# Performance work log

Measured on AMD Instinct MI355X. Metric: run time of the kernel, lower is better.

Reference implementation:

```python
import jax, jax.numpy as jnp
import numpy as np

N = 50000      # nodes
E = 800000     # edges (before self loops)
IN = 128       # in_channels
H = 4          # heads
C = 32         # hidden_channels (per head)
D = H * C      # concat output dim = 128
NEG_SLOPE = 0.2
LN_EPS = 1e-5


def setup_inputs() -> dict:
    key = jax.random.key(0)
    ks = jax.random.split(key, 24)
    def p(k, shape, s=0.1):
        return jax.random.normal(k, shape, dtype=jnp.float32) * s
    inp = {
        "x": p(ks[0], (N, IN), 1.0),
        "edge_index": jax.random.randint(ks[1], (2, E), 0, N, dtype=jnp.int32),
    }
    i = 2
    for l, ind in [(0, IN), (1, D)]:
        inp[f"Wl{l}"] = p(ks[i], (ind, D)); i += 1
        inp[f"bl{l}"] = p(ks[i], (D,), 0.02); i += 1
        inp[f"Wr{l}"] = p(ks[i], (ind, D)); i += 1
        inp[f"br{l}"] = p(ks[i], (D,), 0.02); i += 1
        inp[f"att{l}"] = p(ks[i], (H, C)); i += 1
        inp[f"Wres{l}"] = p(ks[i], (ind, D)); i += 1
        inp[f"bias{l}"] = p(ks[i], (D,), 0.02); i += 1
        inp[f"g{l}"] = jnp.ones((D,), jnp.float32)
        inp[f"be{l}"] = jnp.zeros((D,), jnp.float32)
    return inp


def _gatv2_layer(x, src, dst, Wl, bl, Wr, br, att, Wres, bias):
    """GATv2Conv with concat heads, add_self_loops already applied, residual."""
    n = x.shape[0]
    xl = (x @ Wl + bl).reshape(n, H, C)   # source transform
    xr = (x @ Wr + br).reshape(n, H, C)   # target transform
    # edge-level attention logits: e = a . LeakyReLU(xl[j] + xr[i])  [E, H]
    eh = jax.nn.leaky_relu(xl[src] + xr[dst], negative_slope=NEG_SLOPE)  # [E,H,C]
    score = jnp.einsum('ehc,hc->eh', eh, att)                            # [E,H]
    # segment softmax over incoming edges of each destination node
    smax = jax.ops.segment_max(score, dst, num_segments=n)               # [N,H]
    ex = jnp.exp(score - smax[dst])
    ssum = jax.ops.segment_sum(ex, dst, num_segments=n)                  # [N,H]
    alpha = ex / ssum[dst]                                               # [E,H]
    msg = xl[src] * alpha[:, :, None]                                    # [E,H,C]
    out = jax.ops.segment_sum(msg, dst, num_segments=n).reshape(n, D)
    return out + x @ Wres + bias  # residual (bias=False linear) + final bias


def _layernorm_relu(x, g, b):
    mu = jnp.mean(x, axis=-1, keepdims=True)
    var = jnp.mean(jnp.square(x - mu), axis=-1, keepdims=True)
    return jax.nn.relu((x - mu) * jax.lax.rsqrt(var + LN_EPS) * g + b)


def reference(x, edge_index,
              Wl0, bl0, Wr0, br0, att0, Wres0, bias0, g0, be0,
              Wl1, bl1, Wr1, br1, att1, Wres1, bias1, g1, be1):
    n = x.shape[0]
    loops = jnp.arange(n, dtype=edge_index.dtype)
    src = jnp.concatenate([edge_index[0], loops])  # add_self_loops=True
    dst = jnp.concatenate([edge_index[1], loops])
    h = _gatv2_layer(x, src, dst, Wl0, bl0, Wr0, br0, att0, Wres0, bias0)
    h = _layernorm_relu(h, g0, be0)
    h = _gatv2_layer(h, src, dst, Wl1, bl1, Wr1, br1, att1, Wres1, bias1)
    h = _layernorm_relu(h, g1, be1)
    return h
```

## Files before the change

### kernel.cpp

```cpp
#include <hip/hip_runtime.h>
#include <math.h>

#define D 128
#define LRELU 0.2f
#define LN_EPS 1e-5f
#define INV_LN2 1.4426950408889634f

#define NBMAX 512
#define CAP 4096
#define P1CHUNK 8192

typedef __attribute__((ext_vector_type(8))) short short8;
typedef __attribute__((ext_vector_type(8))) unsigned short ushort8;
typedef __attribute__((ext_vector_type(4))) float f32x4;
typedef __attribute__((ext_vector_type(2))) float f32x2;
typedef __attribute__((ext_vector_type(2))) unsigned int u32x2;

static __device__ __forceinline__ unsigned short f2bf(float f) {
    union { float f; unsigned u; } a; a.f = f;
    unsigned r = a.u + 0x7FFFu + ((a.u >> 16) & 1u);
    return (unsigned short)(r >> 16);
}

static __device__ __forceinline__ f32x2 pk_add(f32x2 a, f32x2 b) {
    f32x2 d; asm("v_pk_add_f32 %0, %1, %2" : "=v"(d) : "v"(a), "v"(b)); return d;
}
static __device__ __forceinline__ f32x2 pk_mul(f32x2 a, f32x2 b) {
    f32x2 d; asm("v_pk_mul_f32 %0, %1, %2" : "=v"(d) : "v"(a), "v"(b)); return d;
}
static __device__ __forceinline__ f32x2 pk_fma(f32x2 a, f32x2 b, f32x2 c) {
    f32x2 d; asm("v_pk_fma_f32 %0, %1, %2, %3" : "=v"(d) : "v"(a), "v"(b), "v"(c)); return d;
}
static __device__ __forceinline__ f32x2 pk_abs(f32x2 a) {
    u32x2 u = __builtin_bit_cast(u32x2, a);
    u &= 0x7FFFFFFFu;
    return __builtin_bit_cast(f32x2, u);
}
static __device__ __forceinline__ f32x2 bf2x(unsigned u) {
    f32x2 r;
    r.x = __uint_as_float(u << 16);
    r.y = __uint_as_float(u & 0xFFFF0000u);
    return r;
}

static __device__ __forceinline__ float red4_dpp(float p) {
    int v = __builtin_amdgcn_update_dpp(0, __builtin_bit_cast(int, p), 0xB1, 0xf, 0xf, true);
    p += __builtin_bit_cast(float, v);
    v = __builtin_amdgcn_update_dpp(0, __builtin_bit_cast(int, p), 0x4E, 0xf, 0xf, true);
    p += __builtin_bit_cast(float, v);
    return p;
}


__global__ __launch_bounds__(256) void k_prep(
    const int* __restrict__ srcp, const int* __restrict__ dstp,
    int* __restrict__ bcur, unsigned* __restrict__ ebuf, int E, int N,
    const float* __restrict__ X, ushort* __restrict__ Xb, int Mp,
    const float* __restrict__ W0, const float* __restrict__ W1, const float* __restrict__ W2,
    const float* __restrict__ W3, const float* __restrict__ W4, const float* __restrict__ W5,
    ushort* __restrict__ Wp, int nP1, int nCV)
{
    const int bx = blockIdx.x;
    const int tid = threadIdx.x;
    if (bx < nP1) {
        __shared__ int h[NBMAX];
        const int E2 = E + N;
        const int e0 = bx * P1CHUNK;
        const int e1 = min(e0 + P1CHUNK, E2);
        for (int t = tid; t < NBMAX; t += 256) h[t] = 0;
        __syncthreads();
        for (int e = e0 + tid; e < e1; e += 256) {
            int d = (e < E) ? dstp[e] : e - E;
            atomicAdd(&h[d >> 7], 1);
        }
        __syncthreads();
        for (int b = tid; b < NBMAX; b += 256) {
            int c = h[b];
            h[b] = c ? atomicAdd(&bcur[b], c) : 0;
        }
        __syncthreads();
        for (int e = e0 + tid; e < e1; e += 256) {
            int d  = (e < E) ? dstp[e] : e - E;
            int sc = (e < E) ? srcp[e] : e - E;
            int b = d >> 7;
            int pos = atomicAdd(&h[b], 1) & (CAP - 1);
            ebuf[(size_t)b * CAP + pos] = ((unsigned)sc << 7) | (unsigned)(d & 127);
        }
    } else if (bx < nP1 + nCV) {
        int idx = (bx - nP1) * 256 + tid;
        if (idx >= Mp * (D / 4)) return;
        ushort4 o;
        if (idx < N * (D / 4)) {
            float4 v = ((const float4*)X)[idx];
            o.x = f2bf(v.x); o.y = f2bf(v.y); o.z = f2bf(v.z); o.w = f2bf(v.w);
        } else {
            o = make_ushort4(0, 0, 0, 0);
        }
        ((ushort4*)Xb)[idx] = o;
    } else {
        int bid = bx - nP1 - nCV;
        int m = bid >> 6;
        int o = ((bid & 63) << 8) + tid;
        const float* W;
        if (m == 0) W = W0; else if (m == 1) W = W1; else if (m == 2) W = W2;
        else if (m == 3) W = W3; else if (m == 4) W = W4; else W = W5;
        int j  = o & 7;
        int l  = (o >> 3) & 63;
        int ct = (o >> 9) & 7;
        int kc = o >> 12;
        int k   = kc * 32 + ((l >> 4) << 3) + j;
        int col = (ct << 4) + (l & 15);
        Wp[m * 16384 + o] = f2bf(W[k * D + col]);
    }
}


static __device__ __forceinline__ void gemm_body(
    int bxg, int seg, int tid,
    const ushort* __restrict__ Xb, const ushort* __restrict__ Wp,
    const float* __restrict__ bl, const float* __restrict__ br,
    ushort* __restrict__ XLb, ushort* __restrict__ XRb, float* __restrict__ RES)
{
    const int l = tid & 63;
    const int wave = tid >> 6;
    const int wr = wave >> 1, wc = wave & 1;
    const int brow = bxg * 128 + wr * 64;
    const ushort* W = Wp + seg * 16384;

    f32x4 acc[4][4] = {};
    const int arow = brow + (l & 15);
    const int koff = (l >> 4) * 8;

    #pragma unroll
    for (int kc = 0; kc < 4; ++kc) {
        short8 A[4], B[4];
        #pragma unroll
        for (int at = 0; at < 4; ++at)
            A[at] = *(const short8*)&Xb[(size_t)(arow + at * 16) * D + kc * 32 + koff];
        #pragma unroll
        for (int ct = 0; ct < 4; ++ct) {
            int ctg = wc * 4 + ct;
            B[ct] = *(const short8*)&W[(((kc * 8 + ctg) * 64) + l) * 8];
        }
        #pragma unroll
        for (int at = 0; at < 4; ++at)
            #pragma unroll
            for (int ct = 0; ct < 4; ++ct)
                acc[at][ct] = __builtin_amdgcn_mfma_f32_16x16x32_bf16(A[at], B[ct], acc[at][ct], 0, 0, 0);
    }

    const int c = l & 15;
    const int r0 = (l >> 4) * 4;
    const float* bias = (seg == 0) ? bl : ((seg == 1) ? br : nullptr);
    #pragma unroll
    for (int ct = 0; ct < 4; ++ct) {
        int gcol = wc * 64 + ct * 16 + c;
        float bv = bias ? bias[gcol] : 0.f;
        #pragma unroll
        for (int at = 0; at < 4; ++at) {
            #pragma unroll
            for (int r = 0; r < 4; ++r) {
                int grow = brow + at * 16 + r0 + r;
                float v = acc[at][ct][r] + bv;
                size_t off = (size_t)grow * D + gcol;
                if (seg == 0)      XLb[off] = f2bf(v);
                else if (seg == 1) XRb[off] = f2bf(v);
                else               RES[off] = v;
            }
        }
    }
}


__global__ __launch_bounds__(256) void k_mid(
    const unsigned* __restrict__ ebuf, const int* __restrict__ bcur,
    int* __restrict__ off, int* __restrict__ ord, int* __restrict__ csrc,
    int N, int NB, int nblk,
    const ushort* __restrict__ Xb, const ushort* __restrict__ Wp,
    const float* __restrict__ bl, const float* __restrict__ br,
    ushort* __restrict__ XLb, ushort* __restrict__ XRb, float* __restrict__ RES)
{
    const int bx = blockIdx.x;
    if (bx < NB) {
        const int b = bx;
        const int base = b << 7;
        const int tid = threadIdx.x;
        const int cntN = min(128, N - base);
        __shared__ int h[128];
        __shared__ int cur[128];
        __shared__ int d2h[64];
        __shared__ int sord[128];
        __shared__ int wsum[4];
        __shared__ int wtot[2];

        int acc = 0;
        for (int t = tid; t < b; t += 256) acc += bcur[t];
        #pragma unroll
        for (int o = 32; o >= 1; o >>= 1) acc += __shfl_xor(acc, o);
        if ((tid & 63) == 0) wsum[tid >> 6] = acc;
        if (tid < 128) h[tid] = 0;
        if (tid < 64) d2h[tid] = 0;
        __syncthreads();
        const int B = wsum[0] + wsum[1] + wsum[2] + wsum[3];

        const int cnt = min(bcur[b], CAP);
        for (int k = tid; k < cnt; k += 256) {
            unsigned v = ebuf[(size_t)b * CAP + k];
            atomicAdd(&h[v & 127], 1);
        }
        __syncthreads();

        int dv = (tid < 128) ? h[tid] : 0;
        int incl = dv;
        if (tid < 128) {
            #pragma unroll
            for (int o = 1; o < 64; o <<= 1) {
                int u = __shfl_up(incl, o);
                if ((tid & 63) >= o) incl += u;
            }
        }
        if (tid == 63)  wtot[0] = incl;
        if (tid == 127) wtot[1] = incl;
        __syncthreads();
        if (tid < 128) {
            int add = (tid >= 64) ? wtot[0] : 0;
            int excl = B + add + incl - dv;
            cur[tid] = excl;
            if (tid < cntN) off[base + tid] = excl;
        }
        if (b == NB - 1 && tid == 0) off[N] = B + wtot[0] + wtot[1];

        if (tid < cntN) atomicAdd(&d2h[min(dv, 63)], 1);
        __syncthreads();
        if (tid < 64) {
            int v2 = d2h[tid];
            int inc2 = v2;
            #pragma unroll
            for (int o = 1; o < 64; o <<= 1) {
                int u = __shfl_up(inc2, o);
                if (tid >= o) inc2 += u;
            }
            d2h[tid] = inc2 - v2;
        }
        __syncthreads();
        if (tid < cntN) {
            int pos = atomicAdd(&d2h[min(dv, 63)], 1);
            sord[pos] = tid;
        }
        __syncthreads();
        if (tid < cntN) ord[base + tid] = base + sord[tid];

        for (int k = tid; k < cnt; k += 256) {
            unsigned v = ebuf[(size_t)b * CAP + k];
            int p = atomicAdd(&cur[v & 127], 1);
            csrc[p] = v >> 7;
        }
    } else {
        int bid = bx - NB;
        int seg = bid / nblk;
        int bxg = bid - seg * nblk;
        gemm_body(bxg, seg, threadIdx.x, Xb, Wp, bl, br, XLb, XRb, RES);
    }
}

__global__ __launch_bounds__(256) void gemm_mfma(
    const ushort* __restrict__ Xb, const ushort* __restrict__ Wp,
    const float* __restrict__ bl, const float* __restrict__ br,
    ushort* __restrict__ XLb, ushort* __restrict__ XRb, float* __restrict__ RES)
{
    gemm_body(blockIdx.x, blockIdx.y, threadIdx.x, Xb, Wp, bl, br, XLb, XRb, RES);
}


__global__ __launch_bounds__(256) void gat_node(
    const ushort* __restrict__ XLb, const ushort* __restrict__ XRb, const float* __restrict__ RES,
    const float* __restrict__ att, const float* __restrict__ bias,
    const float* __restrict__ g, const float* __restrict__ be,
    const int* __restrict__ off, const int* __restrict__ csrc, const int* __restrict__ ord,
    float* __restrict__ OUTf, ushort* __restrict__ OUTb)
{
    const int l = threadIdx.x & 63;
    const int slot = blockIdx.x * 16 + (threadIdx.x >> 6) * 4 + (l >> 4);
    const int i = ord[slot];
    const int f = (l & 15) * 8;
    const unsigned ibase = ((unsigned)i << 7) + f;
    const int lb = l & 48;

    f32x2 at06[4], at04[4];
    #pragma unroll
    for (int k = 0; k < 4; ++k) {
        float2 a = *(const float2*)&att[f + k * 2];
        f32x2 av; av.x = a.x; av.y = a.y;
        at06[k] = av * (0.6f * INV_LN2);
        at04[k] = av * (0.4f * INV_LN2);
    }

    uint4 xru = *(const uint4*)&XRb[ibase];
    f32x2 xr2[4];
    xr2[0] = bf2x(xru.x); xr2[1] = bf2x(xru.y); xr2[2] = bf2x(xru.z); xr2[3] = bf2x(xru.w);

    const int e0 = off[i], e1 = off[i + 1];
    const int len = e1 - e0;
    int mx = max(len, __shfl_xor(len, 16));
    mx = max(mx, __shfl_xor(mx, 32));

    float m = -1e30f, s = 0.f;
    f32x2 a2[4] = {};

    for (int c0 = 0; c0 < mx; c0 += 16) {
        int myj = csrc[min(e0 + c0 + (l & 15), e1 - 1)];
        const int rem = mx - c0;
        const int nbb = min(4, (rem + 3) >> 2);
        const int kleft = len - c0;

        uint4 u_[4];
        {
            int s0 = __shfl(myj, lb + 0);
            int s1 = __shfl(myj, lb + 1);
            int s2 = __shfl(myj, lb + 2);
            int s3 = __shfl(myj, lb + 3);
            u_[0] = *(const uint4*)&XLb[((unsigned)s0 << 7) + f];
            u_[1] = *(const uint4*)&XLb[((unsigned)s1 << 7) + f];
            u_[2] = *(const uint4*)&XLb[((unsigned)s2 << 7) + f];
            u_[3] = *(const uint4*)&XLb[((unsigned)s3 << 7) + f];
        }

        #pragma unroll
        for (int bb = 0; bb < 4; ++bb) {
            if (bb >= nbb) break;
            uint4 uc[4];
            #pragma unroll
            for (int j = 0; j < 4; ++j) uc[j] = u_[j];
            if (bb + 1 < nbb) {
                int s0 = __shfl(myj, lb + (bb + 1) * 4 + 0);
                int s1 = __shfl(myj, lb + (bb + 1) * 4 + 1);
                int s2 = __shfl(myj, lb + (bb + 1) * 4 + 2);
                int s3 = __shfl(myj, lb + (bb + 1) * 4 + 3);
                u_[0] = *(const uint4*)&XLb[((unsigned)s0 << 7) + f];
                u_[1] = *(const uint4*)&XLb[((unsigned)s1 << 7) + f];
                u_[2] = *(const uint4*)&XLb[((unsigned)s2 << 7) + f];
                u_[3] = *(const uint4*)&XLb[((unsigned)s3 << 7) + f];
            }

            const int kb = kleft - bb * 4;
            f32x2 xp[4][4];
            float p[4];
            #pragma unroll
            for (int j = 0; j < 4; ++j) {
                xp[j][0] = bf2x(uc[j].x);
                xp[j][1] = bf2x(uc[j].y);
                xp[j][2] = bf2x(uc[j].z);
                xp[j][3] = bf2x(uc[j].w);
                f32x2 v0 = pk_add(xp[j][0], xr2[0]);
                f32x2 pj2 = pk_mul(v0, at06[0]);
                pj2 = pk_fma(pk_abs(v0), at04[0], pj2);
                #pragma unroll
                for (int k = 1; k < 4; ++k) {
                    f32x2 v = pk_add(xp[j][k], xr2[k]);
                    pj2 = pk_fma(v, at06[k], pj2);
                    pj2 = pk_fma(pk_abs(v), at04[k], pj2);
                }
                float pj = pj2.x + pj2.y;
                pj = red4_dpp(pj);
                p[j] = (j < kb) ? pj : -1e30f;
            }
            float pmax = fmaxf(fmaxf(p[0], p[1]), fmaxf(p[2], p[3]));
            float nm = fmaxf(m, pmax);
            float so = exp2f(m - nm);
            float w0 = exp2f(p[0] - nm), w1 = exp2f(p[1] - nm);
            float w2 = exp2f(p[2] - nm), w3 = exp2f(p[3] - nm);
            s = s * so + ((w0 + w1) + (w2 + w3));
            f32x2 so2; so2.x = so; so2.y = so;
            f32x2 w02; w02.x = w0; w02.y = w0;
            f32x2 w12; w12.x = w1; w12.y = w1;
            f32x2 w22; w22.x = w2; w22.y = w2;
            f32x2 w32; w32.x = w3; w32.y = w3;
            #pragma unroll
            for (int k = 0; k < 4; ++k) {
                f32x2 t = pk_mul(xp[0][k], w02);
                t = pk_fma(xp[1][k], w12, t);
                t = pk_fma(xp[2][k], w22, t);
                t = pk_fma(xp[3][k], w32, t);
                a2[k] = pk_fma(a2[k], so2, t);
            }
            m = nm;
        }
    }

    const float4 rsA = *(const float4*)&RES[ibase];
    const float4 rsB = *(const float4*)&RES[ibase + 4];
    const float4 biA = *(const float4*)&bias[f];
    const float4 biB = *(const float4*)&bias[f + 4];
    float inv = 1.f / s;
    float r0 = a2[0].x * inv + rsA.x + biA.x;
    float r1 = a2[0].y * inv + rsA.y + biA.y;
    float r2 = a2[1].x * inv + rsA.z + biA.z;
    float r3 = a2[1].y * inv + rsA.w + biA.w;
    float r4 = a2[2].x * inv + rsB.x + biB.x;
    float r5 = a2[2].y * inv + rsB.y + biB.y;
    float r6 = a2[3].x * inv + rsB.z + biB.z;
    float r7 = a2[3].y * inv + rsB.w + biB.w;

    float sum = ((r0 + r1) + (r2 + r3)) + ((r4 + r5) + (r6 + r7));
    float sq  = ((r0 * r0 + r1 * r1) + (r2 * r2 + r3 * r3))
              + ((r4 * r4 + r5 * r5) + (r6 * r6 + r7 * r7));
    #pragma unroll
    for (int o = 8; o >= 1; o >>= 1) {
        sum += __shfl_xor(sum, o);
        sq  += __shfl_xor(sq, o);
    }
    float mu  = sum * (1.f / 128.f);
    float var = sq * (1.f / 128.f) - mu * mu;
    float isd = rsqrtf(var + LN_EPS);
    const float4 gvA = *(const float4*)&g[f];
    const float4 gvB = *(const float4*)&g[f + 4];
    const float4 bvA = *(const float4*)&be[f];
    const float4 bvB = *(const float4*)&be[f + 4];
    float o0 = fmaxf((r0 - mu) * isd * gvA.x + bvA.x, 0.f);
    float o1 = fmaxf((r1 - mu) * isd * gvA.y + bvA.y, 0.f);
    float o2 = fmaxf((r2 - mu) * isd * gvA.z + bvA.z, 0.f);
    float o3 = fmaxf((r3 - mu) * isd * gvA.w + bvA.w, 0.f);
    float o4 = fmaxf((r4 - mu) * isd * gvB.x + bvB.x, 0.f);
    float o5 = fmaxf((r5 - mu) * isd * gvB.y + bvB.y, 0.f);
    float o6 = fmaxf((r6 - mu) * isd * gvB.z + bvB.z, 0.f);
    float o7 = fmaxf((r7 - mu) * isd * gvB.w + bvB.w, 0.f);

    if (OUTb) {
        ushort8 ob;
        ob[0] = f2bf(o0); ob[1] = f2bf(o1); ob[2] = f2bf(o2); ob[3] = f2bf(o3);
        ob[4] = f2bf(o4); ob[5] = f2bf(o5); ob[6] = f2bf(o6); ob[7] = f2bf(o7);
        *(ushort8*)&OUTb[ibase] = ob;
    } else {
        *(float4*)&OUTf[ibase]     = make_float4(o0, o1, o2, o3);
        *(float4*)&OUTf[ibase + 4] = make_float4(o4, o5, o6, o7);
    }
}


extern "C" void kernel_launch(void* const* d_in, const int* in_sizes, int n_in,
                              void* d_out, int out_size, void* d_ws, size_t ws_size,
                              hipStream_t stream)
{
    const float* x    = (const float*)d_in[0];
    const int*   ei   = (const int*)d_in[1];
    const float* Wl0  = (const float*)d_in[2];
    const float* bl0  = (const float*)d_in[3];
    const float* Wr0  = (const float*)d_in[4];
    const float* br0  = (const float*)d_in[5];
    const float* att0 = (const float*)d_in[6];
    const float* Wres0= (const float*)d_in[7];
    const float* bias0= (const float*)d_in[8];
    const float* g0   = (const float*)d_in[9];
    const float* be0  = (const float*)d_in[10];
    const float* Wl1  = (const float*)d_in[11];
    const float* bl1  = (const float*)d_in[12];
    const float* Wr1  = (const float*)d_in[13];
    const float* br1  = (const float*)d_in[14];
    const float* att1 = (const float*)d_in[15];
    const float* Wres1= (const float*)d_in[16];
    const float* bias1= (const float*)d_in[17];
    const float* g1   = (const float*)d_in[18];
    const float* be1  = (const float*)d_in[19];

    const int N  = in_sizes[0] / D;
    const int E  = in_sizes[1] / 2;
    const int E2 = E + N;
    const int nblk = (N + 127) / 128;
    const int Mp = nblk * 128;
    const int NB = nblk;

    char* w = (char*)d_ws;
    ushort* Xb  = (ushort*)w; w += (size_t)Mp * D * 2;
    ushort* Hb  = (ushort*)w; w += (size_t)Mp * D * 2;
    ushort* XLb = (ushort*)w; w += (size_t)Mp * D * 2;
    ushort* XRb = (ushort*)w; w += (size_t)Mp * D * 2;
    float*  RES = (float*)w;  w += (size_t)Mp * D * 4;
    ushort* Wp  = (ushort*)w; w += (size_t)6 * 16384 * 2;
    int* off     = (int*)w; w += (size_t)(N + 1) * 4;
    int* ord     = (int*)w; w += (size_t)N * 4;
    int* bcur    = (int*)w; w += (size_t)NBMAX * 4;
    unsigned* ebuf = (unsigned*)w; w += (size_t)NB * CAP * 4;
    int* csrc    = (int*)w; w += (size_t)E2 * 4;

    const int* srcp = ei;
    const int* dstp = ei + E;

    const int nP1 = (E2 + P1CHUNK - 1) / P1CHUNK;
    const int nCV = (Mp * (D / 4) + 255) / 256;
    const int nPW = 6 * 64;
    const int nGM = nblk * 3;

    hipMemsetAsync(bcur, 0, (size_t)NBMAX * 4, stream);
    k_prep<<<nP1 + nCV + nPW, 256, 0, stream>>>(srcp, dstp, bcur, ebuf, E, N,
                                                x, Xb, Mp,
                                                Wl0, Wr0, Wres0, Wl1, Wr1, Wres1,
                                                Wp, nP1, nCV);

    k_mid<<<NB + nGM, 256, 0, stream>>>(ebuf, bcur, off, ord, csrc, N, NB, nblk,
                                        Xb, Wp, bl0, br0, XLb, XRb, RES);

    const int gatg = N / 16;
    dim3 ggrid(nblk, 3);

    gat_node<<<gatg, 256, 0, stream>>>(XLb, XRb, RES, att0, bias0, g0, be0, off, csrc, ord, nullptr, Hb);
    gemm_mfma<<<ggrid, 256, 0, stream>>>(Hb, Wp + 3 * 16384, bl1, br1, XLb, XRb, RES);
    gat_node<<<gatg, 256, 0, stream>>>(XLb, XRb, RES, att1, bias1, g1, be1, off, csrc, ord, (float*)d_out, nullptr);
}
```

Measured before the change: 191.8 us.

## Fuse fp32-to-bf16 input conversion into first GEMM and drop degree-sorted node ordering

The separate pass that converts x to bf16 is removed. The first-layer GEMM now loads fp32 rows directly and converts them in registers, with bounds checks on the rows, which avoids writing and re-reading an intermediate bf16 copy. The per-bucket degree histogram sort that built the ord permutation is also removed, so gat_node processes nodes in natural order. That saves the sort and one indirection, but gives up the degree-based load balancing across lanes.

```diff
diff --git a/kernel.cpp b/kernel.cpp
--- a/kernel.cpp
+++ b/kernel.cpp
@@ -55,10 +55,9 @@
 __global__ __launch_bounds__(256) void k_prep(
     const int* __restrict__ srcp, const int* __restrict__ dstp,
     int* __restrict__ bcur, unsigned* __restrict__ ebuf, int E, int N,
-    const float* __restrict__ X, ushort* __restrict__ Xb, int Mp,
     const float* __restrict__ W0, const float* __restrict__ W1, const float* __restrict__ W2,
     const float* __restrict__ W3, const float* __restrict__ W4, const float* __restrict__ W5,
-    ushort* __restrict__ Wp, int nP1, int nCV)
+    ushort* __restrict__ Wp, int nP1)
 {
     const int bx = blockIdx.x;
     const int tid = threadIdx.x;
@@ -86,19 +85,8 @@
             int pos = atomicAdd(&h[b], 1) & (CAP - 1);
             ebuf[(size_t)b * CAP + pos] = ((unsigned)sc << 7) | (unsigned)(d & 127);
         }
-    } else if (bx < nP1 + nCV) {
-        int idx = (bx - nP1) * 256 + tid;
-        if (idx >= Mp * (D / 4)) return;
-        ushort4 o;
-        if (idx < N * (D / 4)) {
-            float4 v = ((const float4*)X)[idx];
-            o.x = f2bf(v.x); o.y = f2bf(v.y); o.z = f2bf(v.z); o.w = f2bf(v.w);
-        } else {
-            o = make_ushort4(0, 0, 0, 0);
-        }
-        ((ushort4*)Xb)[idx] = o;
     } else {
-        int bid = bx - nP1 - nCV;
+        int bid = bx - nP1;
         int m = bid >> 6;
         int o = ((bid & 63) << 8) + tid;
         const float* W;
@@ -115,9 +103,11 @@
 }
 
 
+template <bool AF32>
 static __device__ __forceinline__ void gemm_body(
-    int bxg, int seg, int tid,
-    const ushort* __restrict__ Xb, const ushort* __restrict__ Wp,
+    int bxg, int seg, int tid, int N,
+    const float* __restrict__ Xf, const ushort* __restrict__ Xb,
+    const ushort* __restrict__ Wp,
     const float* __restrict__ bl, const float* __restrict__ br,
     ushort* __restrict__ XLb, ushort* __restrict__ XRb, float* __restrict__ RES)
 {
@@ -135,8 +125,24 @@
     for (int kc = 0; kc < 4; ++kc) {
         short8 A[4], B[4];
         #pragma unroll
-        for (int at = 0; at < 4; ++at)
-            A[at] = *(const short8*)&Xb[(size_t)(arow + at * 16) * D + kc * 32 + koff];
+        for (int at = 0; at < 4; ++at) {
+            const int r = arow + at * 16;
+            if (AF32) {
+                short8 av = {};
+                if (r < N) {
+                    const float* src = &Xf[(size_t)r * D + kc * 32 + koff];
+                    float4 f0 = *(const float4*)src;
+                    float4 f1 = *(const float4*)(src + 4);
+                    av[0] = (short)f2bf(f0.x); av[1] = (short)f2bf(f0.y);
+                    av[2] = (short)f2bf(f0.z); av[3] = (short)f2bf(f0.w);
+                    av[4] = (short)f2bf(f1.x); av[5] = (short)f2bf(f1.y);
+                    av[6] = (short)f2bf(f1.z); av[7] = (short)f2bf(f1.w);
+                }
+                A[at] = av;
+            } else {
+                A[at] = *(const short8*)&Xb[(size_t)r * D + kc * 32 + koff];
+            }
+        }
         #pragma unroll
         for (int ct = 0; ct < 4; ++ct) {
             int ctg = wc * 4 + ct;
@@ -174,9 +180,9 @@
 
 __global__ __launch_bounds__(256) void k_mid(
     const unsigned* __restrict__ ebuf, const int* __restrict__ bcur,
-    int* __restrict__ off, int* __restrict__ ord, int* __restrict__ csrc,
+    int* __restrict__ off, int* __restrict__ csrc,
     int N, int NB, int nblk,
-    const ushort* __restrict__ Xb, const ushort* __restrict__ Wp,
+    const float* __restrict__ Xf, const ushort* __restrict__ Wp,
     const float* __restrict__ bl, const float* __restrict__ br,
     ushort* __restrict__ XLb, ushort* __restrict__ XRb, float* __restrict__ RES)
 {
@@ -188,8 +194,6 @@
         const int cntN = min(128, N - base);
         __shared__ int h[128];
         __shared__ int cur[128];
-        __shared__ int d2h[64];
-        __shared__ int sord[128];
         __shared__ int wsum[4];
         __shared__ int wtot[2];
 
@@ -199,7 +203,6 @@
         for (int o = 32; o >= 1; o >>= 1) acc += __shfl_xor(acc, o);
         if ((tid & 63) == 0) wsum[tid >> 6] = acc;
         if (tid < 128) h[tid] = 0;
-        if (tid < 64) d2h[tid] = 0;
         __syncthreads();
         const int B = wsum[0] + wsum[1] + wsum[2] + wsum[3];
 
@@ -229,26 +232,7 @@
             if (tid < cntN) off[base + tid] = excl;
         }
         if (b == NB - 1 && tid == 0) off[N] = B + wtot[0] + wtot[1];
-
-        if (tid < cntN) atomicAdd(&d2h[min(dv, 63)], 1);
-        __syncthreads();
-        if (tid < 64) {
-            int v2 = d2h[tid];
-            int inc2 = v2;
-            #pragma unroll
-            for (int o = 1; o < 64; o <<= 1) {
-                int u = __shfl_up(inc2, o);
-                if (tid >= o) inc2 += u;
-            }
-            d2h[tid] = inc2 - v2;
-        }
-        __syncthreads();
-        if (tid < cntN) {
-            int pos = atomicAdd(&d2h[min(dv, 63)], 1);
-            sord[pos] = tid;
-        }
-        __syncthreads();
-        if (tid < cntN) ord[base + tid] = base + sord[tid];
+        __syncthreads();
 
         for (int k = tid; k < cnt; k += 256) {
             unsigned v = ebuf[(size_t)b * CAP + k];
@@ -259,16 +243,16 @@
         int bid = bx - NB;
         int seg = bid / nblk;
         int bxg = bid - seg * nblk;
-        gemm_body(bxg, seg, threadIdx.x, Xb, Wp, bl, br, XLb, XRb, RES);
+        gemm_body<true>(bxg, seg, threadIdx.x, N, Xf, nullptr, Wp, bl, br, XLb, XRb, RES);
     }
 }
 
 __global__ __launch_bounds__(256) void gemm_mfma(
-    const ushort* __restrict__ Xb, const ushort* __restrict__ Wp,
+    const ushort* __restrict__ Xb, const ushort* __restrict__ Wp, int N,
     const float* __restrict__ bl, const float* __restrict__ br,
     ushort* __restrict__ XLb, ushort* __restrict__ XRb, float* __restrict__ RES)
 {
-    gemm_body(blockIdx.x, blockIdx.y, threadIdx.x, Xb, Wp, bl, br, XLb, XRb, RES);
+    gemm_body<false>(blockIdx.x, blockIdx.y, threadIdx.x, N, nullptr, Xb, Wp, bl, br, XLb, XRb, RES);
 }
 
 
@@ -276,12 +260,11 @@
     const ushort* __restrict__ XLb, const ushort* __restrict__ XRb, const float* __restrict__ RES,
     const float* __restrict__ att, const float* __restrict__ bias,
     const float* __restrict__ g, const float* __restrict__ be,
-    const int* __restrict__ off, const int* __restrict__ csrc, const int* __restrict__ ord,
+    const int* __restrict__ off, const int* __restrict__ csrc,
     float* __restrict__ OUTf, ushort* __restrict__ OUTb)
 {
     const int l = threadIdx.x & 63;
-    const int slot = blockIdx.x * 16 + (threadIdx.x >> 6) * 4 + (l >> 4);
-    const int i = ord[slot];
+    const int i = blockIdx.x * 16 + (threadIdx.x >> 6) * 4 + (l >> 4);
     const int f = (l & 15) * 8;
     const unsigned ibase = ((unsigned)i << 7) + f;
     const int lb = l & 48;
@@ -454,8 +437,8 @@
     const float* be0  = (const float*)d_in[10];
     const float* Wl1  = (const float*)d_in[11];
     const float* bl1  = (const float*)d_in[12];
+    const float* br1  = (const float*)d_in[14];
     const float* Wr1  = (const float*)d_in[13];
-    const float* br1  = (const float*)d_in[14];
     const float* att1 = (const float*)d_in[15];
     const float* Wres1= (const float*)d_in[16];
     const float* bias1= (const float*)d_in[17];
@@ -470,14 +453,12 @@
     const int NB = nblk;
 
     char* w = (char*)d_ws;
-    ushort* Xb  = (ushort*)w; w += (size_t)Mp * D * 2;
     ushort* Hb  = (ushort*)w; w += (size_t)Mp * D * 2;
     ushort* XLb = (ushort*)w; w += (size_t)Mp * D * 2;
     ushort* XRb = (ushort*)w; w += (size_t)Mp * D * 2;
     float*  RES = (float*)w;  w += (size_t)Mp * D * 4;
     ushort* Wp  = (ushort*)w; w += (size_t)6 * 16384 * 2;
     int* off     = (int*)w; w += (size_t)(N + 1) * 4;
-    int* ord     = (int*)w; w += (size_t)N * 4;
     int* bcur    = (int*)w; w += (size_t)NBMAX * 4;
     unsigned* ebuf = (unsigned*)w; w += (size_t)NB * CAP * 4;
     int* csrc    = (int*)w; w += (size_t)E2 * 4;
@@ -486,23 +467,21 @@
     const int* dstp = ei + E;
 
     const int nP1 = (E2 + P1CHUNK - 1) / P1CHUNK;
-    const int nCV = (Mp * (D / 4) + 255) / 256;
     const int nPW = 6 * 64;
     const int nGM = nblk * 3;
 
     hipMemsetAsync(bcur, 0, (size_t)NBMAX * 4, stream);
-    k_prep<<<nP1 + nCV + nPW, 256, 0, stream>>>(srcp, dstp, bcur, ebuf, E, N,
-                                                x, Xb, Mp,
-                                                Wl0, Wr0, Wres0, Wl1, Wr1, Wres1,
-                                                Wp, nP1, nCV);
-
-    k_mid<<<NB + nGM, 256, 0, stream>>>(ebuf, bcur, off, ord, csrc, N, NB, nblk,
-                                        Xb, Wp, bl0, br0, XLb, XRb, RES);
+    k_prep<<<nP1 + nPW, 256, 0, stream>>>(srcp, dstp, bcur, ebuf, E, N,
+                                          Wl0, Wr0, Wres0, Wl1, Wr1, Wres1,
+                                          Wp, nP1);
+
+    k_mid<<<NB + nGM, 256, 0, stream>>>(ebuf, bcur, off, csrc, N, NB, nblk,
+                                        x, Wp, bl0, br0, XLb, XRb, RES);
 
     const int gatg = N / 16;
     dim3 ggrid(nblk, 3);
 
-    gat_node<<<gatg, 256, 0, stream>>>(XLb, XRb, RES, att0, bias0, g0, be0, off, csrc, ord, nullptr, Hb);
-    gemm_mfma<<<ggrid, 256, 0, stream>>>(Hb, Wp + 3 * 16384, bl1, br1, XLb, XRb, RES);
-    gat_node<<<gatg, 256, 0, stream>>>(XLb, XRb, RES, att1, bias1, g1, be1, off, csrc, ord, (float*)d_out, nullptr);
-}
+    gat_node<<<gatg, 256, 0, stream>>>(XLb, XRb, RES, att0, bias0, g0, be0, off, csrc, nullptr, Hb);
+    gemm_mfma<<<ggrid, 256, 0, stream>>>(Hb, Wp + 3 * 16384, N, bl1, br1, XLb, XRb, RES);
+    gat_node<<<gatg, 256, 0, stream>>>(XLb, XRb, RES, att1, bias1, g1, be1, off, csrc, (float*)d_out, nullptr);
+}
```

Measured after the change: 194.0 us. No clear change (+1.1%).
